# Kernel tuning notes

Measured on AMD Instinct MI355X. Metric: run time of the kernel, lower is better.

## Reference

```python
import jax, jax.numpy as jnp
import numpy as np

B, D_INPUT, D_MODEL, MEM, HID, N_SYNCH, OUT_DIMS, ITERS = 128, 512, 2048, 25, 32, 256, 1000, 24
SYNC = N_SYNCH * (N_SYNCH + 1) // 2  # 32896


def setup_inputs() -> dict:
    key = jax.random.key(0)
    ks = jax.random.split(key, 12)
    inp = {
        'x': jax.random.normal(ks[0], (B, D_INPUT), jnp.float32),
        'syn_w': jax.random.normal(ks[1], (D_INPUT + D_MODEL, 2 * D_MODEL), jnp.float32) * 0.02,
        'syn_b': jnp.zeros((2 * D_MODEL,), jnp.float32),
        'ln_g': jnp.ones((D_MODEL,), jnp.float32),
        'ln_b': jnp.zeros((D_MODEL,), jnp.float32),
        'tp_w1': jax.random.normal(ks[2], (MEM, 2 * HID, D_MODEL), jnp.float32) * (1.0 / np.sqrt(MEM + 2 * HID)),
        'tp_b1': jnp.zeros((1, D_MODEL, 2 * HID), jnp.float32),
        'tp_w2': jax.random.normal(ks[3], (HID, 2, D_MODEL), jnp.float32) * (1.0 / np.sqrt(HID + 2)),
        'tp_b2': jnp.zeros((1, D_MODEL, 2), jnp.float32),
        'start_activated_state': jax.random.normal(ks[4], (D_MODEL,), jnp.float32) * (1.0 / np.sqrt(D_MODEL)),
        'start_trace': jax.random.normal(ks[5], (D_MODEL, MEM), jnp.float32) * (1.0 / np.sqrt(D_MODEL + MEM)),
        'decay_params_out': jax.random.uniform(ks[6], (SYNC,), jnp.float32),
        'out_w': jax.random.normal(ks[7], (SYNC, OUT_DIMS), jnp.float32) * 0.02,
        'out_b': jnp.zeros((OUT_DIMS,), jnp.float32),
        'idx_left': jax.random.randint(ks[8], (N_SYNCH,), 0, D_MODEL),
        'idx_right': jax.random.randint(ks[9], (N_SYNCH,), 0, D_MODEL),
        'iterations': ITERS,
    }
    return inp


def _glu(z):
    a, b = jnp.split(z, 2, axis=-1)
    return a * jax.nn.sigmoid(b)


def reference(x, syn_w, syn_b, ln_g, ln_b, tp_w1, tp_b1, tp_w2, tp_b2,
              start_activated_state, start_trace, decay_params_out, out_w, out_b,
              idx_left, idx_right, iterations):
    Bx = x.shape[0]
    D, M = start_trace.shape
    n_synch = idx_left.shape[0]
    iu, ju = np.triu_indices(n_synch)
    r = jnp.exp(-jnp.clip(decay_params_out, 0.0, 15.0))[None, :]  # (1, S)
    log_nc = np.log(out_b.shape[0]).astype(np.float32)

    def pairwise(act):  # act: (B, D) -> (B, S) upper-tri of outer product of selected neurons
        l = act[:, idx_left]
        rr = act[:, idx_right]
        outer = l[:, :, None] * rr[:, None, :]
        return outer[:, iu, ju]

    def trace_proc(trace):  # (B, D, M) -> (B, D) per-neuron MLP (NLM)
        h = _glu(jnp.einsum('BDM,MHD->BDH', trace, tp_w1) + tp_b1)
        o = _glu(jnp.einsum('BDH,HOD->BDO', h, tp_w2) + tp_b2)
        return o[..., 0]

    def layernorm(z):
        mu = jnp.mean(z, -1, keepdims=True)
        var = jnp.mean((z - mu) ** 2, -1, keepdims=True)
        return (z - mu) * jax.lax.rsqrt(var + 1e-5) * ln_g + ln_b

    act0 = jnp.broadcast_to(start_activated_state[None, :], (Bx, D))
    trace0 = jnp.broadcast_to(start_trace[None, :, :], (Bx, D, M))
    alpha0 = pairwise(act0)
    beta0 = jnp.ones_like(alpha0)

    def step(carry, _):
        trace, act, alpha, beta = carry
        pre = jnp.concatenate([x, act], axis=-1)
        state = layernorm(_glu(pre @ syn_w + syn_b))            # (B, D)
        trace = jnp.concatenate([trace[:, :, 1:], state[:, :, None]], axis=-1)
        act = trace_proc(trace)                                  # (B, D)
        pp = pairwise(act)
        alpha = r * alpha + pp
        beta = r * beta + 1.0
        sync = alpha / jnp.sqrt(beta)                            # (B, S)
        pred = sync @ out_w + out_b                              # (B, out)
        logp = jax.nn.log_softmax(pred, axis=-1)
        ne = -jnp.sum(jnp.exp(logp) * logp, axis=-1) / log_nc
        cert = jnp.stack([ne, 1.0 - ne], axis=-1)                # (B, 2)
        return (trace, act, alpha, beta), (pred, cert)

    _, (preds, certs) = jax.lax.scan(step, (trace0, act0, alpha0, beta0), None, length=iterations)
    predictions = jnp.moveaxis(preds, 0, -1)   # (B, out_dims, T)
    certainties = jnp.moveaxis(certs, 0, -1)   # (B, 2, T)
    return predictions, certainties
```

## Files before the change

kernel.cpp:

```cpp
#include <hip/hip_runtime.h>
#include <stdint.h>

#define BB      128
#define DIN     512
#define DMODEL  2048
#define MEMN    25
#define NSY     256
#define OUTD    1000
#define ITERS   24
#define SYNCN   32896
#define KPAD    33792
#define NPAD    1024
#define NSPLIT  32
#define KCH     1056
#define PREDTOT (BB*OUTD*ITERS)

typedef __attribute__((ext_vector_type(8))) short bf16x8;
typedef __attribute__((ext_vector_type(4))) float f32x4;

__device__ __forceinline__ unsigned short f2bf(float x){
    unsigned int u = __float_as_uint(x);
    u += 0x7fffu + ((u >> 16) & 1u);
    return (unsigned short)(u >> 16);
}
__device__ __forceinline__ float bf2f(unsigned short h){
    unsigned int u = ((unsigned int)h) << 16;
    return __uint_as_float(u);
}
__device__ __forceinline__ float sigm(float x){ return 1.f/(1.f + __expf(-x)); }

__device__ __forceinline__ void gload16(const unsigned short* g, unsigned short* l){
    __builtin_amdgcn_global_load_lds(
        (const __attribute__((address_space(1))) unsigned int*)(const void*)g,
        (__attribute__((address_space(3))) unsigned int*)(void*)l,
        16, 0, 0);
}


__global__ __launch_bounds__(256) void init_trace_k(const float* __restrict__ st,
    unsigned short* __restrict__ trh, unsigned short* __restrict__ trl){
    const long N = (long)MEMN*DMODEL*BB;
    for (long i = (long)blockIdx.x*256 + threadIdx.x; i < N; i += (long)gridDim.x*256){
        int m = (int)(i / (DMODEL*BB));
        int rem = (int)(i % (DMODEL*BB));
        int d = rem >> 7;
        float v = st[d*MEMN + m];
        unsigned short h = f2bf(v);
        trh[i] = h;
        trl[i] = f2bf(v - bf2f(h));
    }
}

__global__ __launch_bounds__(256) void init_act_k(const float* __restrict__ sas, float* __restrict__ act){
    for (int i = blockIdx.x*256 + threadIdx.x; i < DMODEL*BB; i += gridDim.x*256)
        act[i] = sas[i >> 7];
}

__global__ __launch_bounds__(256) void init_alpha_k(const float* __restrict__ sas,
    const int* __restrict__ il, const int* __restrict__ ir, float* __restrict__ alpha){
    int i = blockIdx.x, tid = threadIdx.x;
    if (tid >= NSY - i) return;
    int j = i + tid;
    int k = i*(2*NSY - i + 1)/2 + tid;
    float a0 = sas[il[i]] * sas[ir[j]];
    for (int b = 0; b < BB; ++b) alpha[b*SYNCN + k] = a0;
}

__global__ __launch_bounds__(256) void init_rowmap_k(int* __restrict__ rowOf, int* __restrict__ rowstart){
    int i = blockIdx.x, tid = threadIdx.x;
    int start = i*(2*NSY - i + 1)/2;
    int len = NSY - i;
    if (tid == 0) rowstart[i] = start;
    for (int t = tid; t < len; t += 256) rowOf[start + t] = i;
}

__global__ __launch_bounds__(256) void transpose_f32_k(const float* __restrict__ in, float* __restrict__ out, int R, int C){
    __shared__ float S[64][65];
    int r0 = blockIdx.y*64, c0 = blockIdx.x*64;
    for (int i = threadIdx.x; i < 64*64; i += 256){
        int rr = i >> 6, cc = i & 63;
        int r = r0+rr, c = c0+cc;
        if (r < R && c < C) S[rr][cc] = in[(long)r*C + c];
    }
    __syncthreads();
    for (int i = threadIdx.x; i < 64*64; i += 256){
        int cc = i >> 6, rr = i & 63;
        int r = r0+rr, c = c0+cc;
        if (r < R && c < C) out[(long)c*R + r] = S[rr][cc];
    }
}

__global__ __launch_bounds__(256) void w1bf_prep_k(const float* __restrict__ w1t, unsigned short* __restrict__ w1bf){
    int d = blockIdx.x, tid = threadIdx.x;
    __shared__ float S[1600];
    for (int i = tid; i < 1600; i += 256) S[i] = w1t[(long)d*1600 + i];
    __syncthreads();
    for (int i = tid; i < 2560; i += 256){
        int h = i/40, m = i - h*40;
        float v = (m < MEMN) ? S[m*64 + h] : 0.f;
        unsigned short hi = f2bf(v);
        unsigned short lo = f2bf(v - bf2f(hi));
        w1bf[(long)d*5120 + i]        = hi;
        w1bf[(long)d*5120 + 2560 + i] = lo;
    }
}

__global__ __launch_bounds__(256) void wbf_transpose_k(const float* __restrict__ w, unsigned short* __restrict__ wt){
    __shared__ float S[64][65];
    int k0 = blockIdx.x*64, n0 = blockIdx.y*64;
    int tid = threadIdx.x;
    if (k0 >= SYNCN){
        uint4 z = {0u,0u,0u,0u};
#pragma unroll
        for (int p = 0; p < 2; ++p){
            int i = tid + p*256;
            int nn = i >> 3, k8 = (i & 7)*8;
            *(uint4*)(wt + (long)(n0+nn)*KPAD + k0 + k8) = z;
        }
        return;
    }
    const long MAXI = (long)SYNCN*OUTD - 4;
#pragma unroll
    for (int p = 0; p < 4; ++p){
        int i = tid + p*256;
        int rr = i >> 4, c4 = (i & 15)*4;
        long idx = (long)(k0+rr)*OUTD + n0 + c4;
        if (idx > MAXI) idx = MAXI;
        float4 v = *(const float4*)(w + idx);
        S[rr][c4+0]=v.x; S[rr][c4+1]=v.y; S[rr][c4+2]=v.z; S[rr][c4+3]=v.w;
    }
    __syncthreads();
#pragma unroll
    for (int p = 0; p < 4; ++p){
        int i = tid + p*256;
        int nn = i >> 4, k4 = (i & 15)*4;
        ushort4 o;
        o.x = f2bf(S[k4+0][nn]); o.y = f2bf(S[k4+1][nn]);
        o.z = f2bf(S[k4+2][nn]); o.w = f2bf(S[k4+3][nn]);
        *(ushort4*)(wt + (long)(n0+nn)*KPAD + k0 + k4) = o;
    }
}

__global__ __launch_bounds__(256) void swt_convert_k(const float* __restrict__ w,
    unsigned short* __restrict__ th, unsigned short* __restrict__ tl){
    __shared__ float S[64][65];
    int k0 = blockIdx.x*64, n0 = blockIdx.y*64;
    int tid = threadIdx.x;
#pragma unroll
    for (int p = 0; p < 4; ++p){
        int i = tid + p*256;
        int rr = i >> 4, c4 = (i & 15)*4;
        float4 v = *(const float4*)(w + (long)(512 + k0 + rr)*4096 + n0 + c4);
        S[rr][c4+0]=v.x; S[rr][c4+1]=v.y; S[rr][c4+2]=v.z; S[rr][c4+3]=v.w;
    }
    __syncthreads();
#pragma unroll
    for (int p = 0; p < 4; ++p){
        int i = tid + p*256;
        int nn = i >> 4, k4 = (i & 15)*4;
        ushort4 oh, ol;
        float v0 = S[k4+0][nn], v1 = S[k4+1][nn], v2 = S[k4+2][nn], v3 = S[k4+3][nn];
        oh.x = f2bf(v0); oh.y = f2bf(v1); oh.z = f2bf(v2); oh.w = f2bf(v3);
        ol.x = f2bf(v0 - bf2f(oh.x)); ol.y = f2bf(v1 - bf2f(oh.y));
        ol.z = f2bf(v2 - bf2f(oh.z)); ol.w = f2bf(v3 - bf2f(oh.w));
        *(ushort4*)(th + (long)(n0+nn)*DMODEL + k0 + k4) = oh;
        *(ushort4*)(tl + (long)(n0+nn)*DMODEL + k0 + k4) = ol;
    }
}

__global__ __launch_bounds__(256) void act_convert_k(const float* __restrict__ act,
    unsigned short* __restrict__ th, unsigned short* __restrict__ tl){
    __shared__ float S[64][65];
    int d0 = blockIdx.x*64, b0 = blockIdx.y*64;
    int tid = threadIdx.x;
#pragma unroll
    for (int p = 0; p < 4; ++p){
        int i = tid + p*256;
        int rr = i >> 4, c4 = (i & 15)*4;
        float4 v = *(const float4*)(act + (long)(d0+rr)*BB + b0 + c4);
        S[rr][c4+0]=v.x; S[rr][c4+1]=v.y; S[rr][c4+2]=v.z; S[rr][c4+3]=v.w;
    }
    __syncthreads();
#pragma unroll
    for (int p = 0; p < 4; ++p){
        int i = tid + p*256;
        int nn = i >> 4, k4 = (i & 15)*4;
        unsigned short h[4], l[4];
#pragma unroll
        for (int q = 0; q < 4; ++q){
            float v = S[k4+q][nn];
            h[q] = f2bf(v);
            l[q] = f2bf(v - bf2f(h[q]));
        }
        *(ushort4*)(th + (long)(b0+nn)*DMODEL + d0 + k4) = ushort4{h[0],h[1],h[2],h[3]};
        *(ushort4*)(tl + (long)(b0+nn)*DMODEL + d0 + k4) = ushort4{l[0],l[1],l[2],l[3]};
    }
}

__global__ __launch_bounds__(256) void gemm_syn_k(const float* __restrict__ A, const float* __restrict__ Bw,
    const float* __restrict__ bias, float* __restrict__ out){
    int j_base = blockIdx.x*64;
    int tid = threadIdx.x;
    __shared__ float As[16][128];
    __shared__ float Bs[16][68];
    int bg = tid & 15, jg = tid >> 4;
    int b0 = bg*8, j0 = jg*4;
    float acc[8][4];
#pragma unroll
    for (int i = 0; i < 8; ++i)
#pragma unroll
        for (int q = 0; q < 4; ++q) acc[i][q] = 0.f;
    for (int kt = 0; kt < 32; ++kt){
        {
            int i0 = tid*8;
            int kk = i0 >> 7, bb = i0 & 127;
            const float4* src = (const float4*)(A + (long)(kt*16+kk)*BB + bb);
            float4 v0 = src[0], v1 = src[1];
            *(float4*)&As[kk][bb]   = v0;
            *(float4*)&As[kk][bb+4] = v1;
        }
        {
            int i0 = tid*4;
            int kk = i0 >> 6, jj = i0 & 63;
            float4 v = *(const float4*)(Bw + (long)(kt*16+kk)*4096 + j_base + jj);
            *(float4*)&Bs[kk][jj] = v;
        }
        __syncthreads();
#pragma unroll
        for (int kk = 0; kk < 16; ++kk){
            float a[8], bv[4];
            *(float4*)&a[0] = *(float4*)&As[kk][b0];
            *(float4*)&a[4] = *(float4*)&As[kk][b0+4];
            *(float4*)&bv[0] = *(float4*)&Bs[kk][j0];
#pragma unroll
            for (int i = 0; i < 8; ++i)
#pragma unroll
                for (int q = 0; q < 4; ++q) acc[i][q] += a[i]*bv[q];
        }
        __syncthreads();
    }
#pragma unroll
    for (int i = 0; i < 8; ++i){
        int bb = b0 + i;
        float4 v;
        v.x = acc[i][0]+bias[j_base+j0+0]; v.y = acc[i][1]+bias[j_base+j0+1];
        v.z = acc[i][2]+bias[j_base+j0+2]; v.w = acc[i][3]+bias[j_base+j0+3];
        *(float4*)(out + (long)bb*4096 + j_base + j0) = v;
    }
}


__global__ __launch_bounds__(256) void syn_mfma_k(const unsigned short* __restrict__ Ah, const unsigned short* __restrict__ Al,
    const unsigned short* __restrict__ Bh, const unsigned short* __restrict__ Bl, float* __restrict__ zpart){
    int nb = blockIdx.x;
    int s  = blockIdx.y;
    int tid = threadIdx.x;
    int wid = tid >> 6, lane = tid & 63;
    int wm = (wid & 1)*64, wn = (wid >> 1)*32;

    __shared__ __align__(16) unsigned short As_h[128*32], As_l[128*32], Bs_h[64*32], Bs_l[64*32];
    f32x4 c[4][2];
#pragma unroll
    for (int a = 0; a < 4; ++a)
#pragma unroll
        for (int b = 0; b < 2; ++b) c[a][b] = (f32x4){0.f,0.f,0.f,0.f};

    int mrow = lane & 15, kq = lane >> 4;
    int srow = tid >> 2;
    int ksg  = (tid & 3)*8;
    long koff0 = (long)s*256 + ksg;
    const unsigned short* gAh1 = Ah + (long)srow*DMODEL      + koff0;
    const unsigned short* gAh2 = Ah + (long)(srow+64)*DMODEL + koff0;
    const unsigned short* gAl1 = Al + (long)srow*DMODEL      + koff0;
    const unsigned short* gAl2 = Al + (long)(srow+64)*DMODEL + koff0;
    const unsigned short* gBh  = Bh + (long)(nb*64+srow)*DMODEL + koff0;
    const unsigned short* gBl  = Bl + (long)(nb*64+srow)*DMODEL + koff0;
    unsigned short* lAh1 = As_h + wid*512;
    unsigned short* lAh2 = As_h + 2048 + wid*512;
    unsigned short* lAl1 = As_l + wid*512;
    unsigned short* lAl2 = As_l + 2048 + wid*512;
    unsigned short* lBh  = Bs_h + wid*512;
    unsigned short* lBl  = Bs_l + wid*512;

    for (int ks = 0; ks < 8; ++ks){
        int o = ks*32;
        gload16(gAh1 + o, lAh1);
        gload16(gAh2 + o, lAh2);
        gload16(gAl1 + o, lAl1);
        gload16(gAl2 + o, lAl2);
        gload16(gBh  + o, lBh);
        gload16(gBl  + o, lBl);
        __syncthreads();
        bf16x8 ah[4], al[4], bh[2], bl[2];
#pragma unroll
        for (int x = 0; x < 4; ++x){
            ah[x] = *(const bf16x8*)&As_h[(wm + x*16 + mrow)*32 + kq*8];
            al[x] = *(const bf16x8*)&As_l[(wm + x*16 + mrow)*32 + kq*8];
        }
#pragma unroll
        for (int y = 0; y < 2; ++y){
            bh[y] = *(const bf16x8*)&Bs_h[(wn + y*16 + mrow)*32 + kq*8];
            bl[y] = *(const bf16x8*)&Bs_l[(wn + y*16 + mrow)*32 + kq*8];
        }
#pragma unroll
        for (int a = 0; a < 4; ++a)
#pragma unroll
            for (int b = 0; b < 2; ++b){
                c[a][b] = __builtin_amdgcn_mfma_f32_16x16x32_bf16(ah[a], bh[b], c[a][b], 0, 0, 0);
                c[a][b] = __builtin_amdgcn_mfma_f32_16x16x32_bf16(al[a], bh[b], c[a][b], 0, 0, 0);
                c[a][b] = __builtin_amdgcn_mfma_f32_16x16x32_bf16(ah[a], bl[b], c[a][b], 0, 0, 0);
            }
        __syncthreads();
    }
    float* outp = zpart + (long)s*(BB*4096);
#pragma unroll
    for (int a = 0; a < 4; ++a)
#pragma unroll
        for (int b = 0; b < 2; ++b){
            int r0 = wm + a*16 + (lane >> 4)*4;
            int col = nb*64 + wn + b*16 + (lane & 15);
#pragma unroll
            for (int reg = 0; reg < 4; ++reg)
                outp[(long)(r0+reg)*4096 + col] = c[a][b][reg];
        }
}

__global__ __launch_bounds__(1024) void glu_ln_k(const float* __restrict__ C0, const float* __restrict__ zp,
    const float* __restrict__ lng, const float* __restrict__ lnb,
    unsigned short* __restrict__ trh, unsigned short* __restrict__ trl, int slot){
    int b = blockIdx.x, tid = threadIdx.x;
    __shared__ float redA[16], redB[16];
    int d0 = tid*2;
    const float* base = C0 + (long)b*4096;
    float2 a = *(const float2*)(base + d0);
    float2 g = *(const float2*)(base + 2048 + d0);
#pragma unroll
    for (int s = 0; s < 8; ++s){
        const float* zb = zp + (long)s*524288 + (long)b*4096;
        float2 az = *(const float2*)(zb + d0);
        float2 gz = *(const float2*)(zb + 2048 + d0);
        a.x += az.x; a.y += az.y; g.x += gz.x; g.y += gz.y;
    }
    float v0 = a.x*sigm(g.x), v1 = a.y*sigm(g.y);
    float s1 = v0+v1, s2 = v0*v0+v1*v1;
#pragma unroll
    for (int off = 32; off; off >>= 1){
        s1 += __shfl_down(s1, off);
        s2 += __shfl_down(s2, off);
    }
    if ((tid & 63) == 0){ redA[tid>>6] = s1; redB[tid>>6] = s2; }
    __syncthreads();
    if (tid == 0){
        float sa = 0.f, sb = 0.f;
        for (int i = 0; i < 16; ++i){ sa += redA[i]; sb += redB[i]; }
        float mu = sa*(1.f/2048.f);
        float var = sb*(1.f/2048.f) - mu*mu;
        redA[0] = mu;
        redB[0] = rsqrtf(var + 1e-5f);
    }
    __syncthreads();
    float mu = redA[0], inv = redB[0];
    float st0 = (v0-mu)*inv*lng[d0]   + lnb[d0];
    float st1 = (v1-mu)*inv*lng[d0+1] + lnb[d0+1];
    unsigned short h0 = f2bf(st0), h1 = f2bf(st1);
    long o0 = ((long)slot*DMODEL + d0)*BB + b;
    trh[o0]      = h0;  trl[o0]      = f2bf(st0 - bf2f(h0));
    trh[o0 + BB] = h1;  trl[o0 + BB] = f2bf(st1 - bf2f(h1));
}

__global__ __launch_bounds__(256) void trace_proc_k(
    const unsigned short* __restrict__ trh, const unsigned short* __restrict__ trl,
    const unsigned short* __restrict__ w1bf,
    const float* __restrict__ b1, const float* __restrict__ w2t, const float* __restrict__ b2,
    float* __restrict__ act, unsigned short* __restrict__ aTh, unsigned short* __restrict__ aTl, int t){
    int d = blockIdx.x, tid = threadIdx.x;
    __shared__ __align__(16) unsigned short Ah[128*40];
    __shared__ __align__(16) unsigned short Al[128*40];
    __shared__ __align__(16) unsigned short Bbuf[5120];
    __shared__ float hh[128*33];
    __shared__ float w2s[64];

    for (int i = tid; i < MEMN*64; i += 256){
        int m = i >> 6, bp = i & 63;
        int phys = t + 1 + m; if (phys >= MEMN) phys -= MEMN; if (phys >= MEMN) phys -= MEMN;
        long gaddr = ((long)phys*DMODEL + d)*BB + bp*2;
        ushort2 vh = *(const ushort2*)(trh + gaddr);
        ushort2 vl = *(const ushort2*)(trl + gaddr);
        Ah[(bp*2+0)*40 + m] = vh.x; Ah[(bp*2+1)*40 + m] = vh.y;
        Al[(bp*2+0)*40 + m] = vl.x; Al[(bp*2+1)*40 + m] = vl.y;
    }
    for (int i = tid; i < 7*128; i += 256){
        int m = MEMN + (i >> 7), b = i & 127;
        Ah[b*40 + m] = 0; Al[b*40 + m] = 0;
    }
    {
        const uint4* src = (const uint4*)(w1bf + (long)d*5120);
        uint4* dst = (uint4*)Bbuf;
        for (int i = tid; i < 640; i += 256) dst[i] = src[i];
    }
    if (tid < 64) w2s[tid] = w2t[(long)d*64 + tid];
    __syncthreads();

    int wid = tid >> 6, lane = tid & 63;
    int mrow = lane & 15, kq = lane >> 4;
    bf16x8 ahf[2], alf[2], bhf[4], blf[4];
#pragma unroll
    for (int bt = 0; bt < 2; ++bt){
        int r = (wid*2 + bt)*16 + mrow;
        ahf[bt] = *(const bf16x8*)&Ah[r*40 + kq*8];
        alf[bt] = *(const bf16x8*)&Al[r*40 + kq*8];
    }
#pragma unroll
    for (int ht = 0; ht < 4; ++ht){
        int r = ht*16 + mrow;
        bhf[ht] = *(const bf16x8*)&Bbuf[r*40 + kq*8];
        blf[ht] = *(const bf16x8*)&Bbuf[2560 + r*40 + kq*8];
    }
    f32x4 c[2][4];
#pragma unroll
    for (int bt = 0; bt < 2; ++bt)
#pragma unroll
        for (int ht = 0; ht < 4; ++ht){
            c[bt][ht] = (f32x4){0.f,0.f,0.f,0.f};
            c[bt][ht] = __builtin_amdgcn_mfma_f32_16x16x32_bf16(ahf[bt], bhf[ht], c[bt][ht], 0, 0, 0);
            c[bt][ht] = __builtin_amdgcn_mfma_f32_16x16x32_bf16(alf[bt], bhf[ht], c[bt][ht], 0, 0, 0);
            c[bt][ht] = __builtin_amdgcn_mfma_f32_16x16x32_bf16(ahf[bt], blf[ht], c[bt][ht], 0, 0, 0);
        }
    int quad = lane >> 4;
#pragma unroll
    for (int bt = 0; bt < 2; ++bt){
        int bb0 = (wid*2 + bt)*16 + quad*4;
#pragma unroll
        for (int ht = 0; ht < 2; ++ht){
            int h = ht*16 + (lane & 15);
            float ba = b1[(long)d*64 + h];
            float bg = b1[(long)d*64 + 32 + h];
#pragma unroll
            for (int reg = 0; reg < 4; ++reg){
                float a = c[bt][ht][reg] + ba;
                float g = c[bt][ht+2][reg] + bg;
                hh[(bb0+reg)*33 + h] = a * sigm(g);
            }
        }
    }
    __syncthreads();
    if (tid < 128){
        int bb = tid;
        float o0 = b2[(long)d*2+0], o1 = b2[(long)d*2+1];
#pragma unroll
        for (int h = 0; h < 32; ++h){
            float hv = hh[bb*33 + h];
            o0 += hv * w2s[h*2+0];
            o1 += hv * w2s[h*2+1];
        }
        float a = o0 * sigm(o1);
        act[(long)d*BB + bb] = a;
        unsigned short h16 = f2bf(a);
        aTh[(long)bb*DMODEL + d] = h16;
        aTl[(long)bb*DMODEL + d] = f2bf(a - bf2f(h16));
    }
}

__global__ __launch_bounds__(256) void pairwise_sync_k(const float* __restrict__ act, const float* __restrict__ decay,
    const int* __restrict__ il, const int* __restrict__ ir,
    const int* __restrict__ rowOf, const int* __restrict__ rowstart,
    float* __restrict__ alpha, unsigned short* __restrict__ syncb, int t){
    int k = blockIdx.x*256 + threadIdx.x;
    int bg = blockIdx.y;
    int blo = bg*32, bhi = blo + 32;
    if (k >= SYNCN){
        if (k < KPAD)
            for (int b = blo; b < bhi; ++b) syncb[(long)b*KPAD + k] = 0;
        return;
    }
    int i = rowOf[k];
    int j = i + (k - rowstart[i]);
    float cc = fminf(fmaxf(decay[k], 0.f), 15.f);
    float r = __expf(-cc);
    float bet;
    if (cc < 1e-30f) bet = (float)(t + 2);
    else {
        float e1 = expm1f(-cc);
        float et = expm1f(-cc*(float)(t+1));
        bet = 1.f + et + et/e1;
    }
    float rs = rsqrtf(bet);
    const float* aL = act + (long)il[i]*BB;
    const float* aR = act + (long)ir[j]*BB;
    for (int b = blo; b < bhi; ++b){
        float pp = aL[b]*aR[b];
        float al = r*alpha[(long)b*SYNCN + k] + pp;
        alpha[(long)b*SYNCN + k] = al;
        syncb[(long)b*KPAD + k] = f2bf(al*rs);
    }
}

__global__ __launch_bounds__(256) void out_gemm_k(const unsigned short* __restrict__ Abf,
    const unsigned short* __restrict__ Bbf, float* __restrict__ part){
    int n_base = blockIdx.x*64;
    int sk = blockIdx.y;
    int tid = threadIdx.x;
    int wid = tid >> 6, lane = tid & 63;
    int wm = (wid & 1)*64, wn = (wid >> 1)*32;
    long k_base = (long)sk*KCH;
    __shared__ __align__(16) unsigned short As[128*32];
    __shared__ __align__(16) unsigned short Bs[64*32];
    f32x4 c[4][2];
#pragma unroll
    for (int a = 0; a < 4; ++a)
#pragma unroll
        for (int b = 0; b < 2; ++b) c[a][b] = (f32x4){0.f,0.f,0.f,0.f};

    int mrow = lane & 15, kq = lane >> 4;
    int srow = tid >> 2;
    int ksg  = (tid & 3)*8;
    const unsigned short* gA1 = Abf + (long)srow*KPAD      + k_base + ksg;
    const unsigned short* gA2 = Abf + (long)(srow+64)*KPAD + k_base + ksg;
    const unsigned short* gB  = Bbf + (long)(n_base+srow)*KPAD + k_base + ksg;
    unsigned short* lA1 = As + wid*512;
    unsigned short* lA2 = As + 2048 + wid*512;
    unsigned short* lB  = Bs + wid*512;

    for (int ks = 0; ks < KCH/32; ++ks){
        int o = ks*32;
        gload16(gA1 + o, lA1);
        gload16(gA2 + o, lA2);
        gload16(gB  + o, lB);
        __syncthreads();
        bf16x8 af[4], bf[2];
#pragma unroll
        for (int x = 0; x < 4; ++x)
            af[x] = *(const bf16x8*)&As[(wm + x*16 + mrow)*32 + kq*8];
#pragma unroll
        for (int y = 0; y < 2; ++y)
            bf[y] = *(const bf16x8*)&Bs[(wn + y*16 + mrow)*32 + kq*8];
#pragma unroll
        for (int a = 0; a < 4; ++a)
#pragma unroll
            for (int b = 0; b < 2; ++b)
                c[a][b] = __builtin_amdgcn_mfma_f32_16x16x32_bf16(af[a], bf[b], c[a][b], 0, 0, 0);
        __syncthreads();
    }
    float* outp = part + (long)sk*(128*NPAD);
#pragma unroll
    for (int a = 0; a < 4; ++a)
#pragma unroll
        for (int b = 0; b < 2; ++b){
            int r0 = wm + a*16 + (lane >> 4)*4;
            int col = n_base + wn + b*16 + (lane & 15);
#pragma unroll
            for (int reg = 0; reg < 4; ++reg)
                outp[(long)(r0+reg)*NPAD + col] = c[a][b][reg];
        }
}

__global__ __launch_bounds__(1024) void reduce_softmax_k(const float* __restrict__ part, const float* __restrict__ outb,
    float* __restrict__ pred_all, float* __restrict__ dout, int t){
    int b = blockIdx.x, tid = threadIdx.x;
    __shared__ float redA[16], redB[16];
    float v = -1e30f;
    if (tid < OUTD){
        float s = outb[tid];
        for (int sk = 0; sk < NSPLIT; ++sk) s += part[(long)sk*(128*NPAD) + (long)b*NPAD + tid];
        v = s;
    }
    float m = v;
#pragma unroll
    for (int off = 32; off; off >>= 1) m = fmaxf(m, __shfl_down(m, off));
    if ((tid & 63) == 0) redA[tid>>6] = m;
    __syncthreads();
    if (tid == 0){
        float r = redA[0];
        for (int i = 1; i < 16; ++i) r = fmaxf(r, redA[i]);
        redA[0] = r;
    }
    __syncthreads();
    float M = redA[0];
    __syncthreads();
    float e  = (tid < OUTD) ? __expf(v - M) : 0.f;
    float ev = e * ((tid < OUTD) ? v : 0.f);
    float z = e, s2 = ev;
#pragma unroll
    for (int off = 32; off; off >>= 1){
        z  += __shfl_down(z, off);
        s2 += __shfl_down(s2, off);
    }
    if ((tid & 63) == 0){ redA[tid>>6] = z; redB[tid>>6] = s2; }
    __syncthreads();
    if (tid == 0){
        float Z = 0.f, S = 0.f;
        for (int i = 0; i < 16; ++i){ Z += redA[i]; S += redB[i]; }
        float logZ = M + __logf(Z);
        float ne = (logZ - S/Z) / 6.907755278982137f;
        dout[PREDTOT + b*48 + t] = ne;
        dout[PREDTOT + b*48 + 24 + t] = 1.f - ne;
    }
    if (tid < OUTD) pred_all[(long)t*(BB*OUTD) + (long)b*OUTD + tid] = v;
}

__global__ __launch_bounds__(256) void transpose_pred_k(const float* __restrict__ pa, float* __restrict__ dout){
    int b = blockIdx.x;
    int n0 = blockIdx.y*64;
    __shared__ float S[64][25];
    for (int i = threadIdx.x; i < 24*64; i += 256){
        int tt = i >> 6, j = i & 63;
        int n = n0 + j;
        if (n < OUTD) S[j][tt] = pa[(long)tt*(BB*OUTD) + (long)b*OUTD + n];
    }
    __syncthreads();
    for (int i = threadIdx.x; i < 64*24; i += 256){
        int j = i / 24, tt = i % 24;
        int n = n0 + j;
        if (n < OUTD) dout[(long)b*(OUTD*ITERS) + (long)n*ITERS + tt] = S[j][tt];
    }
}


extern "C" void kernel_launch(void* const* d_in, const int* in_sizes, int n_in,
                              void* d_out, int out_size, void* d_ws, size_t ws_size,
                              hipStream_t stream){
    const float* x      = (const float*)d_in[0];
    const float* syn_w  = (const float*)d_in[1];
    const float* syn_b  = (const float*)d_in[2];
    const float* ln_g   = (const float*)d_in[3];
    const float* ln_b   = (const float*)d_in[4];
    const float* tp_w1  = (const float*)d_in[5];
    const float* tp_b1  = (const float*)d_in[6];
    const float* tp_w2  = (const float*)d_in[7];
    const float* tp_b2  = (const float*)d_in[8];
    const float* sas    = (const float*)d_in[9];
    const float* strc   = (const float*)d_in[10];
    const float* decay  = (const float*)d_in[11];
    const float* out_w  = (const float*)d_in[12];
    const float* out_b  = (const float*)d_in[13];
    const int*   il     = (const int*)d_in[14];
    const int*   ir     = (const int*)d_in[15];
    float* dout = (float*)d_out;

    char* ws = (char*)d_ws;
    size_t off = 0;
    auto alloc = [&](size_t bytes)->void*{
        void* p = ws + off;
        off += (bytes + 255) & ~(size_t)255;
        return p;
    };
    unsigned short* trh = (unsigned short*)alloc((size_t)MEMN*DMODEL*BB*2);
    unsigned short* trl = (unsigned short*)alloc((size_t)MEMN*DMODEL*BB*2);
    float* act     = (float*)alloc((size_t)DMODEL*BB*4);
    float* C0      = (float*)alloc((size_t)BB*4096*4);
    float* xt      = (float*)alloc((size_t)DIN*BB*4);
    float* w2t     = (float*)alloc((size_t)DMODEL*64*4);
    unsigned short* w1bf = (unsigned short*)alloc((size_t)DMODEL*5120*2);
    float* alpha   = (float*)alloc((size_t)BB*SYNCN*4);
    unsigned short* syncb = (unsigned short*)alloc((size_t)BB*KPAD*2);
    unsigned short* wbt   = (unsigned short*)alloc((size_t)NPAD*KPAD*2);
    float* pred_all= (float*)alloc((size_t)ITERS*BB*OUTD*4);
    float* shared_big = (float*)alloc((size_t)NSPLIT*BB*NPAD*4);
    float* w1t   = shared_big;
    float* zpart = shared_big;
    float* part  = shared_big;
    unsigned short* swT_h = (unsigned short*)alloc((size_t)4096*DMODEL*2);
    unsigned short* swT_l = (unsigned short*)alloc((size_t)4096*DMODEL*2);
    unsigned short* aT_h  = (unsigned short*)alloc((size_t)BB*DMODEL*2);
    unsigned short* aT_l  = (unsigned short*)alloc((size_t)BB*DMODEL*2);
    int* rowOf    = (int*)alloc((size_t)SYNCN*4);
    int* rowstart = (int*)alloc((size_t)NSY*4);
    (void)ws_size; (void)in_sizes; (void)n_in; (void)out_size;

    init_trace_k<<<8192, 256, 0, stream>>>(strc, trh, trl);
    init_act_k<<<1024, 256, 0, stream>>>(sas, act);
    init_alpha_k<<<256, 256, 0, stream>>>(sas, il, ir, alpha);
    init_rowmap_k<<<256, 256, 0, stream>>>(rowOf, rowstart);
    transpose_f32_k<<<dim3(32, 25), 256, 0, stream>>>(tp_w1, w1t, 1600, 2048);
    w1bf_prep_k<<<2048, 256, 0, stream>>>(w1t, w1bf);
    transpose_f32_k<<<dim3(32, 1),  256, 0, stream>>>(tp_w2, w2t, 64, 2048);
    transpose_f32_k<<<dim3(8, 2),   256, 0, stream>>>(x, xt, 128, 512);
    wbf_transpose_k<<<dim3(KPAD/64, 16), 256, 0, stream>>>(out_w, wbt);
    swt_convert_k<<<dim3(32, 64), 256, 0, stream>>>(syn_w, swT_h, swT_l);
    gemm_syn_k<<<64, 256, 0, stream>>>(xt, syn_w, syn_b, C0);
    act_convert_k<<<dim3(32, 2), 256, 0, stream>>>(act, aT_h, aT_l);

    for (int t = 0; t < ITERS; ++t){
        syn_mfma_k<<<dim3(64, 8), 256, 0, stream>>>(aT_h, aT_l, swT_h, swT_l, zpart);
        glu_ln_k<<<128, 1024, 0, stream>>>(C0, zpart, ln_g, ln_b, trh, trl, t % MEMN);
        trace_proc_k<<<2048, 256, 0, stream>>>(trh, trl, w1bf, tp_b1, w2t, tp_b2, act, aT_h, aT_l, t);
        pairwise_sync_k<<<dim3(KPAD/256, 4), 256, 0, stream>>>(act, decay, il, ir, rowOf, rowstart, alpha, syncb, t);
        out_gemm_k<<<dim3(16, NSPLIT), 256, 0, stream>>>(syncb, wbt, part);
        reduce_softmax_k<<<128, 1024, 0, stream>>>(part, out_b, pred_all, dout, t);
    }
    transpose_pred_k<<<dim3(128, 16), 256, 0, stream>>>(pred_all, dout);
}
```

Measured before the change: 2.728 ms.

## Double-buffer GEMM tiles, fold softmax reduction into next syn kernel, drop pred transpose

Adds LDS double buffering to syn_mfma_k and out_gemm_k, so the next K-slice is loaded while the current one is multiplied and one barrier per step is removed. The per-step reduce_softmax kernel becomes an extra row of blocks in the next iteration's syn_mfma launch, with a final reduce after the loop. Predictions are written straight to the output layout, which removes the pred_all buffer and the transpose kernel. It also shrinks the trace_proc K padding from 40 to 32. The price is separate zpart and part buffers, more LDS per block, and strided scattered output writes.

```diff
diff --git a/kernel.cpp b/kernel.cpp
--- a/kernel.cpp
+++ b/kernel.cpp
@@ -36,6 +36,60 @@
         16, 0, 0);
 }
 
+__device__ __forceinline__ void reduce_row(const float* __restrict__ part, const float* __restrict__ outb,
+    float* __restrict__ dout, float* red, int b, int t, int tid){
+    float v[4];
+    float m = -1e30f;
+#pragma unroll
+    for (int q = 0; q < 4; ++q){
+        int n = q*256 + tid;
+        float s;
+        if (n < OUTD){
+            s = outb[n];
+            for (int sk = 0; sk < NSPLIT; ++sk)
+                s += part[(long)sk*(BB*NPAD) + (long)b*NPAD + n];
+        } else s = -1e30f;
+        v[q] = s;
+        m = fmaxf(m, s);
+    }
+#pragma unroll
+    for (int off = 32; off; off >>= 1) m = fmaxf(m, __shfl_down(m, off));
+    int w = tid >> 6;
+    if ((tid & 63) == 0) red[w] = m;
+    __syncthreads();
+    float M = fmaxf(fmaxf(red[0], red[1]), fmaxf(red[2], red[3]));
+    __syncthreads();
+    float z = 0.f, s2 = 0.f;
+#pragma unroll
+    for (int q = 0; q < 4; ++q){
+        int n = q*256 + tid;
+        if (n < OUTD){
+            float e = __expf(v[q] - M);
+            z += e; s2 += e*v[q];
+        }
+    }
+#pragma unroll
+    for (int off = 32; off; off >>= 1){
+        z  += __shfl_down(z, off);
+        s2 += __shfl_down(s2, off);
+    }
+    if ((tid & 63) == 0){ red[w] = z; red[4+w] = s2; }
+    __syncthreads();
+    if (tid == 0){
+        float Z = red[0]+red[1]+red[2]+red[3];
+        float S = red[4]+red[5]+red[6]+red[7];
+        float logZ = M + __logf(Z);
+        float ne = (logZ - S/Z) / 6.907755278982137f;
+        dout[PREDTOT + b*48 + t] = ne;
+        dout[PREDTOT + b*48 + 24 + t] = 1.f - ne;
+    }
+#pragma unroll
+    for (int q = 0; q < 4; ++q){
+        int n = q*256 + tid;
+        if (n < OUTD) dout[(long)b*(OUTD*ITERS) + (long)n*ITERS + t] = v[q];
+    }
+}
+
 
 __global__ __launch_bounds__(256) void init_trace_k(const float* __restrict__ st,
     unsigned short* __restrict__ trh, unsigned short* __restrict__ trl){
@@ -95,13 +149,13 @@
     __shared__ float S[1600];
     for (int i = tid; i < 1600; i += 256) S[i] = w1t[(long)d*1600 + i];
     __syncthreads();
-    for (int i = tid; i < 2560; i += 256){
-        int h = i/40, m = i - h*40;
+    for (int i = tid; i < 2048; i += 256){
+        int h = i >> 5, m = i & 31;
         float v = (m < MEMN) ? S[m*64 + h] : 0.f;
         unsigned short hi = f2bf(v);
         unsigned short lo = f2bf(v - bf2f(hi));
-        w1bf[(long)d*5120 + i]        = hi;
-        w1bf[(long)d*5120 + 2560 + i] = lo;
+        w1bf[(long)d*4096 + i]        = hi;
+        w1bf[(long)d*4096 + 2048 + i] = lo;
     }
 }
 
@@ -251,14 +305,26 @@
 
 
 __global__ __launch_bounds__(256) void syn_mfma_k(const unsigned short* __restrict__ Ah, const unsigned short* __restrict__ Al,
-    const unsigned short* __restrict__ Bh, const unsigned short* __restrict__ Bl, float* __restrict__ zpart){
+    const unsigned short* __restrict__ Bh, const unsigned short* __restrict__ Bl, float* __restrict__ zpart,
+    const float* __restrict__ part, const float* __restrict__ outb, float* __restrict__ dout, int tprev){
+    __shared__ __align__(16) unsigned short As_h[2][128*32], As_l[2][128*32], Bs_h[2][64*32], Bs_l[2][64*32];
+    __shared__ float red[8];
+    int tid = threadIdx.x;
+
+    if (blockIdx.y == 8){
+        if (tprev >= 0){
+            reduce_row(part, outb, dout, red, 2*blockIdx.x,   tprev, tid);
+            __syncthreads();
+            reduce_row(part, outb, dout, red, 2*blockIdx.x+1, tprev, tid);
+        }
+        return;
+    }
+
     int nb = blockIdx.x;
     int s  = blockIdx.y;
-    int tid = threadIdx.x;
     int wid = tid >> 6, lane = tid & 63;
     int wm = (wid & 1)*64, wn = (wid >> 1)*32;
 
-    __shared__ __align__(16) unsigned short As_h[128*32], As_l[128*32], Bs_h[64*32], Bs_l[64*32];
     f32x4 c[4][2];
 #pragma unroll
     for (int a = 0; a < 4; ++a)
@@ -275,32 +341,36 @@
     const unsigned short* gAl2 = Al + (long)(srow+64)*DMODEL + koff0;
     const unsigned short* gBh  = Bh + (long)(nb*64+srow)*DMODEL + koff0;
     const unsigned short* gBl  = Bl + (long)(nb*64+srow)*DMODEL + koff0;
-    unsigned short* lAh1 = As_h + wid*512;
-    unsigned short* lAh2 = As_h + 2048 + wid*512;
-    unsigned short* lAl1 = As_l + wid*512;
-    unsigned short* lAl2 = As_l + 2048 + wid*512;
-    unsigned short* lBh  = Bs_h + wid*512;
-    unsigned short* lBl  = Bs_l + wid*512;
-
+
+    gload16(gAh1, &As_h[0][wid*512]);
+    gload16(gAh2, &As_h[0][2048 + wid*512]);
+    gload16(gAl1, &As_l[0][wid*512]);
+    gload16(gAl2, &As_l[0][2048 + wid*512]);
+    gload16(gBh , &Bs_h[0][wid*512]);
+    gload16(gBl , &Bs_l[0][wid*512]);
+    __syncthreads();
     for (int ks = 0; ks < 8; ++ks){
-        int o = ks*32;
-        gload16(gAh1 + o, lAh1);
-        gload16(gAh2 + o, lAh2);
-        gload16(gAl1 + o, lAl1);
-        gload16(gAl2 + o, lAl2);
-        gload16(gBh  + o, lBh);
-        gload16(gBl  + o, lBl);
-        __syncthreads();
+        int cur = ks & 1;
+        if (ks < 7){
+            int nxt = cur ^ 1;
+            int o = (ks+1)*32;
+            gload16(gAh1 + o, &As_h[nxt][wid*512]);
+            gload16(gAh2 + o, &As_h[nxt][2048 + wid*512]);
+            gload16(gAl1 + o, &As_l[nxt][wid*512]);
+            gload16(gAl2 + o, &As_l[nxt][2048 + wid*512]);
+            gload16(gBh  + o, &Bs_h[nxt][wid*512]);
+            gload16(gBl  + o, &Bs_l[nxt][wid*512]);
+        }
         bf16x8 ah[4], al[4], bh[2], bl[2];
 #pragma unroll
         for (int x = 0; x < 4; ++x){
-            ah[x] = *(const bf16x8*)&As_h[(wm + x*16 + mrow)*32 + kq*8];
-            al[x] = *(const bf16x8*)&As_l[(wm + x*16 + mrow)*32 + kq*8];
+            ah[x] = *(const bf16x8*)&As_h[cur][(wm + x*16 + mrow)*32 + kq*8];
+            al[x] = *(const bf16x8*)&As_l[cur][(wm + x*16 + mrow)*32 + kq*8];
         }
 #pragma unroll
         for (int y = 0; y < 2; ++y){
-            bh[y] = *(const bf16x8*)&Bs_h[(wn + y*16 + mrow)*32 + kq*8];
-            bl[y] = *(const bf16x8*)&Bs_l[(wn + y*16 + mrow)*32 + kq*8];
+            bh[y] = *(const bf16x8*)&Bs_h[cur][(wn + y*16 + mrow)*32 + kq*8];
+            bl[y] = *(const bf16x8*)&Bs_l[cur][(wn + y*16 + mrow)*32 + kq*8];
         }
 #pragma unroll
         for (int a = 0; a < 4; ++a)
@@ -374,9 +444,9 @@
     const float* __restrict__ b1, const float* __restrict__ w2t, const float* __restrict__ b2,
     float* __restrict__ act, unsigned short* __restrict__ aTh, unsigned short* __restrict__ aTl, int t){
     int d = blockIdx.x, tid = threadIdx.x;
-    __shared__ __align__(16) unsigned short Ah[128*40];
-    __shared__ __align__(16) unsigned short Al[128*40];
-    __shared__ __align__(16) unsigned short Bbuf[5120];
+    __shared__ __align__(16) unsigned short Ah[128*32];
+    __shared__ __align__(16) unsigned short Al[128*32];
+    __shared__ __align__(16) unsigned short Bbuf[4096];
     __shared__ float hh[128*33];
     __shared__ float w2s[64];
 
@@ -386,17 +456,17 @@
         long gaddr = ((long)phys*DMODEL + d)*BB + bp*2;
         ushort2 vh = *(const ushort2*)(trh + gaddr);
         ushort2 vl = *(const ushort2*)(trl + gaddr);
-        Ah[(bp*2+0)*40 + m] = vh.x; Ah[(bp*2+1)*40 + m] = vh.y;
-        Al[(bp*2+0)*40 + m] = vl.x; Al[(bp*2+1)*40 + m] = vl.y;
+        Ah[(bp*2+0)*32 + m] = vh.x; Ah[(bp*2+1)*32 + m] = vh.y;
+        Al[(bp*2+0)*32 + m] = vl.x; Al[(bp*2+1)*32 + m] = vl.y;
     }
     for (int i = tid; i < 7*128; i += 256){
         int m = MEMN + (i >> 7), b = i & 127;
-        Ah[b*40 + m] = 0; Al[b*40 + m] = 0;
+        Ah[b*32 + m] = 0; Al[b*32 + m] = 0;
     }
     {
-        const uint4* src = (const uint4*)(w1bf + (long)d*5120);
+        const uint4* src = (const uint4*)(w1bf + (long)d*4096);
         uint4* dst = (uint4*)Bbuf;
-        for (int i = tid; i < 640; i += 256) dst[i] = src[i];
+        for (int i = tid; i < 512; i += 256) dst[i] = src[i];
     }
     if (tid < 64) w2s[tid] = w2t[(long)d*64 + tid];
     __syncthreads();
@@ -407,14 +477,14 @@
 #pragma unroll
     for (int bt = 0; bt < 2; ++bt){
         int r = (wid*2 + bt)*16 + mrow;
-        ahf[bt] = *(const bf16x8*)&Ah[r*40 + kq*8];
-        alf[bt] = *(const bf16x8*)&Al[r*40 + kq*8];
+        ahf[bt] = *(const bf16x8*)&Ah[r*32 + kq*8];
+        alf[bt] = *(const bf16x8*)&Al[r*32 + kq*8];
     }
 #pragma unroll
     for (int ht = 0; ht < 4; ++ht){
         int r = ht*16 + mrow;
-        bhf[ht] = *(const bf16x8*)&Bbuf[r*40 + kq*8];
-        blf[ht] = *(const bf16x8*)&Bbuf[2560 + r*40 + kq*8];
+        bhf[ht] = *(const bf16x8*)&Bbuf[r*32 + kq*8];
+        blf[ht] = *(const bf16x8*)&Bbuf[2048 + r*32 + kq*8];
     }
     f32x4 c[2][4];
 #pragma unroll
@@ -503,8 +573,8 @@
     int wid = tid >> 6, lane = tid & 63;
     int wm = (wid & 1)*64, wn = (wid >> 1)*32;
     long k_base = (long)sk*KCH;
-    __shared__ __align__(16) unsigned short As[128*32];
-    __shared__ __align__(16) unsigned short Bs[64*32];
+    __shared__ __align__(16) unsigned short As[2][128*32];
+    __shared__ __align__(16) unsigned short Bs[2][64*32];
     f32x4 c[4][2];
 #pragma unroll
     for (int a = 0; a < 4; ++a)
@@ -517,23 +587,28 @@
     const unsigned short* gA1 = Abf + (long)srow*KPAD      + k_base + ksg;
     const unsigned short* gA2 = Abf + (long)(srow+64)*KPAD + k_base + ksg;
     const unsigned short* gB  = Bbf + (long)(n_base+srow)*KPAD + k_base + ksg;
-    unsigned short* lA1 = As + wid*512;
-    unsigned short* lA2 = As + 2048 + wid*512;
-    unsigned short* lB  = Bs + wid*512;
-
-    for (int ks = 0; ks < KCH/32; ++ks){
-        int o = ks*32;
-        gload16(gA1 + o, lA1);
-        gload16(gA2 + o, lA2);
-        gload16(gB  + o, lB);
-        __syncthreads();
+
+    const int NS = KCH/32;
+    gload16(gA1, &As[0][wid*512]);
+    gload16(gA2, &As[0][2048 + wid*512]);
+    gload16(gB , &Bs[0][wid*512]);
+    __syncthreads();
+    for (int ks = 0; ks < NS; ++ks){
+        int cur = ks & 1;
+        if (ks < NS-1){
+            int nxt = cur ^ 1;
+            int o = (ks+1)*32;
+            gload16(gA1 + o, &As[nxt][wid*512]);
+            gload16(gA2 + o, &As[nxt][2048 + wid*512]);
+            gload16(gB  + o, &Bs[nxt][wid*512]);
+        }
         bf16x8 af[4], bf[2];
 #pragma unroll
         for (int x = 0; x < 4; ++x)
-            af[x] = *(const bf16x8*)&As[(wm + x*16 + mrow)*32 + kq*8];
+            af[x] = *(const bf16x8*)&As[cur][(wm + x*16 + mrow)*32 + kq*8];
 #pragma unroll
         for (int y = 0; y < 2; ++y)
-            bf[y] = *(const bf16x8*)&Bs[(wn + y*16 + mrow)*32 + kq*8];
+            bf[y] = *(const bf16x8*)&Bs[cur][(wn + y*16 + mrow)*32 + kq*8];
 #pragma unroll
         for (int a = 0; a < 4; ++a)
 #pragma unroll
@@ -554,65 +629,10 @@
         }
 }
 
-__global__ __launch_bounds__(1024) void reduce_softmax_k(const float* __restrict__ part, const float* __restrict__ outb,
-    float* __restrict__ pred_all, float* __restrict__ dout, int t){
-    int b = blockIdx.x, tid = threadIdx.x;
-    __shared__ float redA[16], redB[16];
-    float v = -1e30f;
-    if (tid < OUTD){
-        float s = outb[tid];
-        for (int sk = 0; sk < NSPLIT; ++sk) s += part[(long)sk*(128*NPAD) + (long)b*NPAD + tid];
-        v = s;
-    }
-    float m = v;
-#pragma unroll
-    for (int off = 32; off; off >>= 1) m = fmaxf(m, __shfl_down(m, off));
-    if ((tid & 63) == 0) redA[tid>>6] = m;
-    __syncthreads();
-    if (tid == 0){
-        float r = redA[0];
-        for (int i = 1; i < 16; ++i) r = fmaxf(r, redA[i]);
-        redA[0] = r;
-    }
-    __syncthreads();
-    float M = redA[0];
-    __syncthreads();
-    float e  = (tid < OUTD) ? __expf(v - M) : 0.f;
-    float ev = e * ((tid < OUTD) ? v : 0.f);
-    float z = e, s2 = ev;
-#pragma unroll
-    for (int off = 32; off; off >>= 1){
-        z  += __shfl_down(z, off);
-        s2 += __shfl_down(s2, off);
-    }
-    if ((tid & 63) == 0){ redA[tid>>6] = z; redB[tid>>6] = s2; }
-    __syncthreads();
-    if (tid == 0){
-        float Z = 0.f, S = 0.f;
-        for (int i = 0; i < 16; ++i){ Z += redA[i]; S += redB[i]; }
-        float logZ = M + __logf(Z);
-        float ne = (logZ - S/Z) / 6.907755278982137f;
-        dout[PREDTOT + b*48 + t] = ne;
-        dout[PREDTOT + b*48 + 24 + t] = 1.f - ne;
-    }
-    if (tid < OUTD) pred_all[(long)t*(BB*OUTD) + (long)b*OUTD + tid] = v;
-}
-
-__global__ __launch_bounds__(256) void transpose_pred_k(const float* __restrict__ pa, float* __restrict__ dout){
-    int b = blockIdx.x;
-    int n0 = blockIdx.y*64;
-    __shared__ float S[64][25];
-    for (int i = threadIdx.x; i < 24*64; i += 256){
-        int tt = i >> 6, j = i & 63;
-        int n = n0 + j;
-        if (n < OUTD) S[j][tt] = pa[(long)tt*(BB*OUTD) + (long)b*OUTD + n];
-    }
-    __syncthreads();
-    for (int i = threadIdx.x; i < 64*24; i += 256){
-        int j = i / 24, tt = i % 24;
-        int n = n0 + j;
-        if (n < OUTD) dout[(long)b*(OUTD*ITERS) + (long)n*ITERS + tt] = S[j][tt];
-    }
+__global__ __launch_bounds__(256) void reduce_final_k(const float* __restrict__ part,
+    const float* __restrict__ outb, float* __restrict__ dout){
+    __shared__ float red[8];
+    reduce_row(part, outb, dout, red, blockIdx.x, ITERS-1, threadIdx.x);
 }
 
 
@@ -650,15 +670,13 @@
     float* C0      = (float*)alloc((size_t)BB*4096*4);
     float* xt      = (float*)alloc((size_t)DIN*BB*4);
     float* w2t     = (float*)alloc((size_t)DMODEL*64*4);
-    unsigned short* w1bf = (unsigned short*)alloc((size_t)DMODEL*5120*2);
+    unsigned short* w1bf = (unsigned short*)alloc((size_t)DMODEL*4096*2);
     float* alpha   = (float*)alloc((size_t)BB*SYNCN*4);
     unsigned short* syncb = (unsigned short*)alloc((size_t)BB*KPAD*2);
     unsigned short* wbt   = (unsigned short*)alloc((size_t)NPAD*KPAD*2);
-    float* pred_all= (float*)alloc((size_t)ITERS*BB*OUTD*4);
-    float* shared_big = (float*)alloc((size_t)NSPLIT*BB*NPAD*4);
-    float* w1t   = shared_big;
-    float* zpart = shared_big;
-    float* part  = shared_big;
+    float* part    = (float*)alloc((size_t)NSPLIT*BB*NPAD*4);
+    float* w1t     = part;
+    float* zpart   = (float*)alloc((size_t)8*BB*4096*4);
     unsigned short* swT_h = (unsigned short*)alloc((size_t)4096*DMODEL*2);
     unsigned short* swT_l = (unsigned short*)alloc((size_t)4096*DMODEL*2);
     unsigned short* aT_h  = (unsigned short*)alloc((size_t)BB*DMODEL*2);
@@ -681,12 +699,12 @@
     act_convert_k<<<dim3(32, 2), 256, 0, stream>>>(act, aT_h, aT_l);
 
     for (int t = 0; t < ITERS; ++t){
-        syn_mfma_k<<<dim3(64, 8), 256, 0, stream>>>(aT_h, aT_l, swT_h, swT_l, zpart);
+        syn_mfma_k<<<dim3(64, 9), 256, 0, stream>>>(aT_h, aT_l, swT_h, swT_l, zpart,
+                                                    part, out_b, dout, t - 1);
         glu_ln_k<<<128, 1024, 0, stream>>>(C0, zpart, ln_g, ln_b, trh, trl, t % MEMN);
         trace_proc_k<<<2048, 256, 0, stream>>>(trh, trl, w1bf, tp_b1, w2t, tp_b2, act, aT_h, aT_l, t);
         pairwise_sync_k<<<dim3(KPAD/256, 4), 256, 0, stream>>>(act, decay, il, ir, rowOf, rowstart, alpha, syncb, t);
         out_gemm_k<<<dim3(16, NSPLIT), 256, 0, stream>>>(syncb, wbt, part);
-        reduce_softmax_k<<<128, 1024, 0, stream>>>(part, out_b, pred_all, dout, t);
-    }
-    transpose_pred_k<<<dim3(128, 16), 256, 0, stream>>>(pred_all, dout);
-}
+    }
+    reduce_final_k<<<128, 256, 0, stream>>>(part, out_b, dout);
+}
```

Measured after the change: 3.029 ms. +11.1%, slower.
